# Kernel optimization log

Measured on AMD Instinct MI355X. Metric: run time of the kernel, lower is better.

Reference implementation:

```python
import jax, jax.numpy as jnp
import numpy as np

HIDDEN = 1024
HEADS = 16
HEAD_DIM = HIDDEN // HEADS


def setup_inputs() -> dict:
    key = jax.random.key(0)
    ks = jax.random.split(key, 7)
    B, S = 4, 2048
    xav = float(np.sqrt(6.0 / (HIDDEN + HIDDEN)))  # xavier uniform bound
    def lin(k):
        return jax.random.uniform(k, (HIDDEN, HIDDEN), jnp.float32, -xav, xav)
    return {
        "hidden_states": jax.random.normal(ks[0], (B, S, HIDDEN), jnp.float32),
        "Wq": lin(ks[1]), "bq": jnp.zeros((HIDDEN,), jnp.float32),
        "Wk": lin(ks[2]), "bk": jnp.zeros((HIDDEN,), jnp.float32),
        "Wv": lin(ks[3]), "bv": jnp.zeros((HIDDEN,), jnp.float32),
    }


def reference(hidden_states, Wq, bq, Wk, bk, Wv, bv):
    B, S, H = hidden_states.shape
    def split_heads(t):  # [B,S,H] -> [B,heads,S,head_dim]
        return t.reshape(B, S, HEADS, HEAD_DIM).transpose(0, 2, 1, 3)
    q = split_heads(hidden_states @ Wq + bq)
    k = split_heads(hidden_states @ Wk + bk)
    v = split_heads(hidden_states @ Wv + bv)
    scores = jnp.einsum("bhqd,bhkd->bhqk", q, k) / jnp.sqrt(
        jnp.asarray(HEAD_DIM, hidden_states.dtype))
    probs = jax.nn.softmax(scores, axis=-1)  # dropout p=0.0 (inference)
    ctx = jnp.einsum("bhqk,bhkd->bhqd", probs, v)
    ctx = ctx.transpose(0, 2, 1, 3).reshape(B, S, H)
    return ctx
```

## Files before the change

kernel.cpp:

```cpp
#include <hip/hip_runtime.h>
#include <hip/hip_bf16.h>
#include <cstdint>

#define HIDDEN 1024
#define HEADS 16
#define HDIM 64
#define BATCH 4
#define SEQ 2048
#define MTOT (BATCH * SEQ)

typedef __attribute__((ext_vector_type(8))) short bfrag;
typedef __attribute__((ext_vector_type(4))) float cfrag;
typedef __attribute__((ext_vector_type(4))) float float4v;
typedef __attribute__((ext_vector_type(4))) unsigned short ushort4v;
typedef __attribute__((ext_vector_type(2))) unsigned int uint2v;

#define AS1 __attribute__((address_space(1)))
#define AS3 __attribute__((address_space(3)))

__device__ __forceinline__ void gl_lds16(const void* g, void* l) {
  __builtin_amdgcn_global_load_lds((AS1 void*)g, (AS3 void*)l, 16, 0, 0);
}

__device__ __forceinline__ uint16_t f2b(float f) {
  union { float f; uint32_t u; } v; v.f = f;
  uint32_t u = v.u;
  return (uint16_t)((u + 0x7FFFu + ((u >> 16) & 1u)) >> 16);
}

__global__ __launch_bounds__(256) void cvt_x_kernel(const float* __restrict__ in,
                                                    uint16_t* __restrict__ out, int n8) {
  int i = blockIdx.x * blockDim.x + threadIdx.x;
  if (i >= n8) return;
  float4v a = ((const float4v*)in)[2 * i];
  float4v b = ((const float4v*)in)[2 * i + 1];
  bfrag o;
  o[0] = (short)f2b(a[0]); o[1] = (short)f2b(a[1]);
  o[2] = (short)f2b(a[2]); o[3] = (short)f2b(a[3]);
  o[4] = (short)f2b(b[0]); o[5] = (short)f2b(b[1]);
  o[6] = (short)f2b(b[2]); o[7] = (short)f2b(b[3]);
  ((bfrag*)out)[i] = o;
}

__global__ __launch_bounds__(256) void cvt_w_kernel(const float* __restrict__ W0,
                                                    const float* __restrict__ W1,
                                                    const float* __restrict__ W2,
                                                    uint16_t* __restrict__ Wt) {
  const float* W = blockIdx.z == 0 ? W0 : (blockIdx.z == 1 ? W1 : W2);
  uint16_t* out = Wt + (size_t)blockIdx.z * HIDDEN * HIDDEN;
  __shared__ float tile[64][65];
  int n0 = blockIdx.x * 64, k0 = blockIdx.y * 64;
  int t = threadIdx.x;
  int r = t >> 2, cq = (t & 3) * 16;
#pragma unroll
  for (int i = 0; i < 16; i += 4) {
    float4v v = *(const float4v*)&W[(size_t)(k0 + r) * HIDDEN + n0 + cq + i];
    tile[r][cq + i + 0] = v[0]; tile[r][cq + i + 1] = v[1];
    tile[r][cq + i + 2] = v[2]; tile[r][cq + i + 3] = v[3];
  }
  __syncthreads();
  bfrag o0, o1;
#pragma unroll
  for (int i = 0; i < 8; ++i) o0[i] = (short)f2b(tile[cq + i][r]);
#pragma unroll
  for (int i = 0; i < 8; ++i) o1[i] = (short)f2b(tile[cq + 8 + i][r]);
  *(bfrag*)&out[(size_t)(n0 + r) * HIDDEN + k0 + cq] = o0;
  *(bfrag*)&out[(size_t)(n0 + r) * HIDDEN + k0 + cq + 8] = o1;
}

__global__ __launch_bounds__(256) void gemm_qkv_kernel(
    const uint16_t* __restrict__ X, const uint16_t* __restrict__ Wt,
    const float* __restrict__ b0, const float* __restrict__ b1,
    const float* __restrict__ b2,
    uint16_t* __restrict__ Qo, uint16_t* __restrict__ Ko, uint16_t* __restrict__ Vo) {
  __shared__ uint16_t As[128 * 32];
  __shared__ uint16_t Bs[128 * 32];

  int id = blockIdx.x;
  int xcd = id & 7, j = id >> 3;
  int which = j >> 6;
  int r_ = j & 63;
  int m0 = (xcd * 8 + (r_ >> 3)) * 128;
  int n0 = (r_ & 7) * 128;

  const uint16_t* Wp = Wt + (size_t)which * HIDDEN * HIDDEN;
  const float* bias = which == 0 ? b0 : (which == 1 ? b1 : b2);

  int tid = threadIdx.x;
  int wave = tid >> 6, lane = tid & 63;
  int wm = wave >> 1, wn = wave & 1;
  int g = lane >> 4, c = lane & 15;
  int sr = lane >> 2;
  int sc = (lane & 3) * 8;

  cfrag acc[4][4];
#pragma unroll
  for (int i = 0; i < 4; ++i)
#pragma unroll
    for (int jj = 0; jj < 4; ++jj) acc[i][jj] = cfrag{0.f, 0.f, 0.f, 0.f};

  for (int kt = 0; kt < HIDDEN / 32; ++kt) {
    int kc = kt * 32 + sc;
#pragma unroll
    for (int i = 0; i < 2; ++i) {
      int rowA = (i * 4 + wave) * 16;
      gl_lds16(&X[(size_t)(m0 + rowA + sr) * HIDDEN + kc], &As[rowA * 32]);
      gl_lds16(&Wp[(size_t)(n0 + rowA + sr) * HIDDEN + kc], &Bs[rowA * 32]);
    }
    __syncthreads();
    bfrag af[4], bf[4];
#pragma unroll
    for (int mt = 0; mt < 4; ++mt)
      af[mt] = *(const bfrag*)&As[(wm * 64 + mt * 16 + c) * 32 + g * 8];
#pragma unroll
    for (int nt = 0; nt < 4; ++nt)
      bf[nt] = *(const bfrag*)&Bs[(wn * 64 + nt * 16 + c) * 32 + g * 8];
#pragma unroll
    for (int mt = 0; mt < 4; ++mt)
#pragma unroll
      for (int nt = 0; nt < 4; ++nt)
        acc[mt][nt] = __builtin_amdgcn_mfma_f32_16x16x32_bf16(af[mt], bf[nt],
                                                              acc[mt][nt], 0, 0, 0);
    __syncthreads();
  }

  if (which == 2) {
    int bb_ = m0 >> 11;
    int s0 = (m0 & 2047) + wm * 64;
#pragma unroll
    for (int nt = 0; nt < 4; ++nt) {
      int n = n0 + wn * 64 + nt * 16 + c;
      int h = n >> 6, d = n & 63;
      float bb = bias[n];
      size_t base = ((size_t)(bb_ * 16 + h) * 64 + d) * SEQ;
#pragma unroll
      for (int mt = 0; mt < 4; ++mt) {
        int s = s0 + mt * 16 + g * 4;
        ushort4v pk;
        pk[0] = f2b(acc[mt][nt][0] + bb);
        pk[1] = f2b(acc[mt][nt][1] + bb);
        pk[2] = f2b(acc[mt][nt][2] + bb);
        pk[3] = f2b(acc[mt][nt][3] + bb);
        *(ushort4v*)&Vo[base + s] = pk;
      }
    }
  } else {
    uint16_t* out = which == 0 ? Qo : Ko;
    float sc_ = which == 0 ? 0.125f * 1.44269504088896f : 1.0f;
#pragma unroll
    for (int nt = 0; nt < 4; ++nt) {
      int n = n0 + wn * 64 + nt * 16 + c;
      float bb = bias[n];
#pragma unroll
      for (int mt = 0; mt < 4; ++mt) {
        int mb = m0 + wm * 64 + mt * 16 + g * 4;
#pragma unroll
        for (int r = 0; r < 4; ++r)
          out[(size_t)(mb + r) * HIDDEN + n] = f2b((acc[mt][nt][r] + bb) * sc_);
      }
    }
  }
}

__global__ __launch_bounds__(256, 4) void attn_kernel(
    const uint16_t* __restrict__ Q, const uint16_t* __restrict__ K,
    const uint16_t* __restrict__ VT, float* __restrict__ out) {
  __shared__ uint16_t Ks[2][64 * 64];
  __shared__ uint16_t Vs[2][64 * 64];
  __shared__ __align__(16) uint16_t Pl[4][16][64];

  int bid = blockIdx.x;
  int wg = (bid & 7) * 256 + (bid >> 3);
  int bh = wg >> 5, qt = wg & 31;
  int b = bh >> 4, h = bh & 15;
  int tid = threadIdx.x, wave = tid >> 6, lane = tid & 63;
  int g = lane >> 4, c = lane & 15;
  size_t rowb = (size_t)b * SEQ;
  int colb = h * HDIM;
  const uint16_t* Kh = K + rowb * HIDDEN + colb;
  const uint16_t* Vh = VT + (size_t)bh * HDIM * SEQ;

  int r8 = lane >> 3, c8 = lane & 7;
  int scol = ((c8 ^ r8) << 3);
  int sbrow = (wave & 1) * 32;

  int qrow = qt * 64 + wave * 16 + c;
  bfrag aq[2];
  aq[0] = *(const bfrag*)&Q[(rowb + qrow) * HIDDEN + colb + g * 8];
  aq[1] = *(const bfrag*)&Q[(rowb + qrow) * HIDDEN + colb + 32 + g * 8];

  float mr = -INFINITY, lr = 0.f;
  cfrag oacc[4];
#pragma unroll
  for (int dt = 0; dt < 4; ++dt) oacc[dt] = cfrag{0.f, 0.f, 0.f, 0.f};

  if (wave < 2) {
#pragma unroll
    for (int j = 0; j < 4; ++j) {
      int rl = sbrow + j * 8;
      gl_lds16(&Kh[(size_t)(rl + r8) * HIDDEN + scol], &Ks[0][rl * 64]);
    }
  } else {
#pragma unroll
    for (int j = 0; j < 4; ++j) {
      int rl = sbrow + j * 8;
      gl_lds16(&Vh[(size_t)(rl + r8) * SEQ + scol], &Vs[0][rl * 64]);
    }
  }
  __syncthreads();

  int cur = 0;
  int sw = (c & 7) << 4;
  uint8_t* Pb = (uint8_t*)Pl + wave * 2048 + c * 128;

  for (int t = 0; t < 32; ++t) {
    int j0 = t * 64;
    if (t < 31) {
      int jn = j0 + 64;
      if (wave < 2) {
#pragma unroll
        for (int j = 0; j < 4; ++j) {
          int rl = sbrow + j * 8;
          gl_lds16(&Kh[(size_t)(jn + rl + r8) * HIDDEN + scol],
                   &Ks[cur ^ 1][rl * 64]);
        }
      } else {
#pragma unroll
        for (int j = 0; j < 4; ++j) {
          int rl = sbrow + j * 8;
          gl_lds16(&Vh[(size_t)(rl + r8) * SEQ + jn + scol],
                   &Vs[cur ^ 1][rl * 64]);
        }
      }
    }

    const uint8_t* Kbuf = (const uint8_t*)Ks[cur];
    const uint8_t* Vbuf = (const uint8_t*)Vs[cur];

    cfrag s[4];
#pragma unroll
    for (int nt = 0; nt < 4; ++nt) s[nt] = cfrag{0.f, 0.f, 0.f, 0.f};
    __builtin_amdgcn_s_setprio(1);
#pragma unroll
    for (int kb = 0; kb < 2; ++kb) {
#pragma unroll
      for (int nt = 0; nt < 4; ++nt) {
        int off = ((nt * 16 + c) * 128 + kb * 64 + g * 16) ^ sw;
        bfrag bk = *(const bfrag*)(Kbuf + off);
        s[nt] = __builtin_amdgcn_mfma_f32_16x16x32_bf16(bk, aq[kb], s[nt], 0, 0, 0);
      }
    }
    __builtin_amdgcn_s_setprio(0);

    float mx = fmaxf(fmaxf(fmaxf(s[0][0], s[0][1]), s[0][2]), s[0][3]);
    float mx1 = fmaxf(fmaxf(fmaxf(s[1][0], s[1][1]), s[1][2]), s[1][3]);
    float mx2 = fmaxf(fmaxf(fmaxf(s[2][0], s[2][1]), s[2][2]), s[2][3]);
    float mx3 = fmaxf(fmaxf(fmaxf(s[3][0], s[3][1]), s[3][2]), s[3][3]);
    mx = fmaxf(fmaxf(mx, mx1), fmaxf(mx2, mx3));
    mx = fmaxf(mx, __shfl_xor(mx, 16, 64));
    mx = fmaxf(mx, __shfl_xor(mx, 32, 64));
    if (mx > mr + 8.0f) {
      float alpha = __builtin_amdgcn_exp2f(mr - mx);
      lr *= alpha;
#pragma unroll
      for (int dt = 0; dt < 4; ++dt)
#pragma unroll
        for (int r = 0; r < 4; ++r) oacc[dt][r] *= alpha;
      mr = mx;
    }
    float ps = 0.f;
#pragma unroll
    for (int nt = 0; nt < 4; ++nt) {
#pragma unroll
      for (int r = 0; r < 4; ++r)
        s[nt][r] = __builtin_amdgcn_exp2f(s[nt][r] - mr);
      ps += (s[nt][0] + s[nt][1]) + (s[nt][2] + s[nt][3]);
    }
    lr += ps;

#pragma unroll
    for (int nt = 0; nt < 4; ++nt) {
      uint32_t w0, w1;
      asm("v_cvt_pk_bf16_f32 %0, %1, %2" : "=v"(w0) : "v"(s[nt][0]), "v"(s[nt][1]));
      asm("v_cvt_pk_bf16_f32 %0, %1, %2" : "=v"(w1) : "v"(s[nt][2]), "v"(s[nt][3]));
      uint2v pw; pw[0] = w0; pw[1] = w1;
      *(uint2v*)(Pb + ((nt * 32 + g * 8) ^ sw)) = pw;
    }

    __builtin_amdgcn_s_setprio(1);
#pragma unroll
    for (int kb = 0; kb < 2; ++kb) {
      bfrag ap = *(const bfrag*)(Pb + ((kb * 64 + g * 16) ^ sw));
#pragma unroll
      for (int dt = 0; dt < 4; ++dt) {
        int off = ((dt * 16 + c) * 128 + kb * 64 + g * 16) ^ sw;
        bfrag bv = *(const bfrag*)(Vbuf + off);
        oacc[dt] = __builtin_amdgcn_mfma_f32_16x16x32_bf16(bv, ap, oacc[dt], 0, 0, 0);
      }
    }
    __builtin_amdgcn_s_setprio(0);

    __syncthreads();
    cur ^= 1;
  }

  lr += __shfl_xor(lr, 16, 64);
  lr += __shfl_xor(lr, 32, 64);
  float inv = 1.0f / lr;
  size_t orow = rowb + (size_t)qt * 64 + wave * 16 + c;
#pragma unroll
  for (int dt = 0; dt < 4; ++dt) {
    float4v o;
    o[0] = oacc[dt][0] * inv; o[1] = oacc[dt][1] * inv;
    o[2] = oacc[dt][2] * inv; o[3] = oacc[dt][3] * inv;
    *(float4v*)&out[orow * HIDDEN + colb + dt * 16 + g * 4] = o;
  }
}

extern "C" void kernel_launch(void* const* d_in, const int* in_sizes, int n_in,
                              void* d_out, int out_size, void* d_ws, size_t ws_size,
                              hipStream_t stream) {
  const float* x  = (const float*)d_in[0];
  const float* Wq = (const float*)d_in[1];
  const float* bq = (const float*)d_in[2];
  const float* Wk = (const float*)d_in[3];
  const float* bk = (const float*)d_in[4];
  const float* Wv = (const float*)d_in[5];
  const float* bv = (const float*)d_in[6];
  float* out = (float*)d_out;

  uint8_t* ws = (uint8_t*)d_ws;
  const size_t XB = 0;
  const size_t WT = XB + (size_t)MTOT * HIDDEN * 2;
  const size_t QB = WT + (size_t)3 * HIDDEN * HIDDEN * 2;
  const size_t KB = QB + (size_t)MTOT * HIDDEN * 2;
  const size_t VB = KB + (size_t)MTOT * HIDDEN * 2;
  uint16_t* Xb = (uint16_t*)(ws + XB);
  uint16_t* Wt = (uint16_t*)(ws + WT);
  uint16_t* Qb = (uint16_t*)(ws + QB);
  uint16_t* Kb = (uint16_t*)(ws + KB);
  uint16_t* Vb = (uint16_t*)(ws + VB);

  cvt_x_kernel<<<dim3(MTOT * HIDDEN / 8 / 256), 256, 0, stream>>>(x, Xb,
                                                                  MTOT * HIDDEN / 8);
  cvt_w_kernel<<<dim3(16, 16, 3), 256, 0, stream>>>(Wq, Wk, Wv, Wt);
  gemm_qkv_kernel<<<dim3(1536), 256, 0, stream>>>(Xb, Wt, bq, bk, bv, Qb, Kb, Vb);
  attn_kernel<<<dim3(2048), 256, 0, stream>>>(Qb, Kb, Vb, out);
}
```

Before: 277.0 us.

## Merge conversion kernels, double-buffer QKV GEMM LDS, restructure softmax max reduction

The two fp32-to-bf16 conversion kernels are merged into one launch that picks its role by block index, removing one kernel launch and its tail. The QKV GEMM now double-buffers its LDS tiles, issuing the next k-tile's global-to-LDS load before computing on the current one, and raises wave priority around the MFMA block. The attention row-max is rewritten as a serial fmax chain. The double buffering doubles the GEMM's LDS use, which may lower occupancy. It also relies on one barrier per iteration to order the asynchronous LDS loads, which could be fragile.

Result: slower. 284.7 us (+2.8%).

```diff
diff --git a/kernel.cpp b/kernel.cpp
--- a/kernel.cpp
+++ b/kernel.cpp
@@ -28,28 +28,29 @@
   return (uint16_t)((u + 0x7FFFu + ((u >> 16) & 1u)) >> 16);
 }
 
-__global__ __launch_bounds__(256) void cvt_x_kernel(const float* __restrict__ in,
-                                                    uint16_t* __restrict__ out, int n8) {
-  int i = blockIdx.x * blockDim.x + threadIdx.x;
-  if (i >= n8) return;
-  float4v a = ((const float4v*)in)[2 * i];
-  float4v b = ((const float4v*)in)[2 * i + 1];
-  bfrag o;
-  o[0] = (short)f2b(a[0]); o[1] = (short)f2b(a[1]);
-  o[2] = (short)f2b(a[2]); o[3] = (short)f2b(a[3]);
-  o[4] = (short)f2b(b[0]); o[5] = (short)f2b(b[1]);
-  o[6] = (short)f2b(b[2]); o[7] = (short)f2b(b[3]);
-  ((bfrag*)out)[i] = o;
-}
-
-__global__ __launch_bounds__(256) void cvt_w_kernel(const float* __restrict__ W0,
-                                                    const float* __restrict__ W1,
-                                                    const float* __restrict__ W2,
-                                                    uint16_t* __restrict__ Wt) {
-  const float* W = blockIdx.z == 0 ? W0 : (blockIdx.z == 1 ? W1 : W2);
-  uint16_t* out = Wt + (size_t)blockIdx.z * HIDDEN * HIDDEN;
+__global__ __launch_bounds__(256) void cvt_kernel(
+    const float* __restrict__ x, const float* __restrict__ W0,
+    const float* __restrict__ W1, const float* __restrict__ W2,
+    uint16_t* __restrict__ Xb, uint16_t* __restrict__ Wt) {
+  int bid = blockIdx.x;
+  if (bid < 4096) {
+    int i = bid * 256 + threadIdx.x;
+    float4v a = ((const float4v*)x)[2 * i];
+    float4v b = ((const float4v*)x)[2 * i + 1];
+    bfrag o;
+    o[0] = (short)f2b(a[0]); o[1] = (short)f2b(a[1]);
+    o[2] = (short)f2b(a[2]); o[3] = (short)f2b(a[3]);
+    o[4] = (short)f2b(b[0]); o[5] = (short)f2b(b[1]);
+    o[6] = (short)f2b(b[2]); o[7] = (short)f2b(b[3]);
+    ((bfrag*)Xb)[i] = o;
+    return;
+  }
+  int id = bid - 4096;
+  int z = id >> 8, rem = id & 255;
+  const float* W = z == 0 ? W0 : (z == 1 ? W1 : W2);
+  uint16_t* out = Wt + (size_t)z * HIDDEN * HIDDEN;
   __shared__ float tile[64][65];
-  int n0 = blockIdx.x * 64, k0 = blockIdx.y * 64;
+  int n0 = (rem & 15) * 64, k0 = (rem >> 4) * 64;
   int t = threadIdx.x;
   int r = t >> 2, cq = (t & 3) * 16;
 #pragma unroll
@@ -73,8 +74,8 @@
     const float* __restrict__ b0, const float* __restrict__ b1,
     const float* __restrict__ b2,
     uint16_t* __restrict__ Qo, uint16_t* __restrict__ Ko, uint16_t* __restrict__ Vo) {
-  __shared__ uint16_t As[128 * 32];
-  __shared__ uint16_t Bs[128 * 32];
+  __shared__ uint16_t As[2][128 * 32];
+  __shared__ uint16_t Bs[2][128 * 32];
 
   int id = blockIdx.x;
   int xcd = id & 7, j = id >> 3;
@@ -99,29 +100,39 @@
 #pragma unroll
     for (int jj = 0; jj < 4; ++jj) acc[i][jj] = cfrag{0.f, 0.f, 0.f, 0.f};
 
-  for (int kt = 0; kt < HIDDEN / 32; ++kt) {
+  auto STAGE = [&](int buf, int kt) {
     int kc = kt * 32 + sc;
 #pragma unroll
     for (int i = 0; i < 2; ++i) {
       int rowA = (i * 4 + wave) * 16;
-      gl_lds16(&X[(size_t)(m0 + rowA + sr) * HIDDEN + kc], &As[rowA * 32]);
-      gl_lds16(&Wp[(size_t)(n0 + rowA + sr) * HIDDEN + kc], &Bs[rowA * 32]);
-    }
-    __syncthreads();
+      gl_lds16(&X[(size_t)(m0 + rowA + sr) * HIDDEN + kc], &As[buf][rowA * 32]);
+      gl_lds16(&Wp[(size_t)(n0 + rowA + sr) * HIDDEN + kc], &Bs[buf][rowA * 32]);
+    }
+  };
+
+  STAGE(0, 0);
+  __syncthreads();
+  int cur = 0;
+
+  for (int kt = 0; kt < HIDDEN / 32; ++kt) {
+    if (kt < HIDDEN / 32 - 1) STAGE(cur ^ 1, kt + 1);
     bfrag af[4], bf[4];
 #pragma unroll
     for (int mt = 0; mt < 4; ++mt)
-      af[mt] = *(const bfrag*)&As[(wm * 64 + mt * 16 + c) * 32 + g * 8];
+      af[mt] = *(const bfrag*)&As[cur][(wm * 64 + mt * 16 + c) * 32 + g * 8];
 #pragma unroll
     for (int nt = 0; nt < 4; ++nt)
-      bf[nt] = *(const bfrag*)&Bs[(wn * 64 + nt * 16 + c) * 32 + g * 8];
+      bf[nt] = *(const bfrag*)&Bs[cur][(wn * 64 + nt * 16 + c) * 32 + g * 8];
+    __builtin_amdgcn_s_setprio(1);
 #pragma unroll
     for (int mt = 0; mt < 4; ++mt)
 #pragma unroll
       for (int nt = 0; nt < 4; ++nt)
         acc[mt][nt] = __builtin_amdgcn_mfma_f32_16x16x32_bf16(af[mt], bf[nt],
                                                               acc[mt][nt], 0, 0, 0);
+    __builtin_amdgcn_s_setprio(0);
     __syncthreads();
+    cur ^= 1;
   }
 
   if (which == 2) {
@@ -252,11 +263,14 @@
     }
     __builtin_amdgcn_s_setprio(0);
 
-    float mx = fmaxf(fmaxf(fmaxf(s[0][0], s[0][1]), s[0][2]), s[0][3]);
-    float mx1 = fmaxf(fmaxf(fmaxf(s[1][0], s[1][1]), s[1][2]), s[1][3]);
-    float mx2 = fmaxf(fmaxf(fmaxf(s[2][0], s[2][1]), s[2][2]), s[2][3]);
-    float mx3 = fmaxf(fmaxf(fmaxf(s[3][0], s[3][1]), s[3][2]), s[3][3]);
-    mx = fmaxf(fmaxf(mx, mx1), fmaxf(mx2, mx3));
+    float mx = fmaxf(fmaxf(s[0][0], s[0][1]), s[0][2]);
+    mx = fmaxf(fmaxf(mx, s[0][3]), s[1][0]);
+    mx = fmaxf(fmaxf(mx, s[1][1]), s[1][2]);
+    mx = fmaxf(fmaxf(mx, s[1][3]), s[2][0]);
+    mx = fmaxf(fmaxf(mx, s[2][1]), s[2][2]);
+    mx = fmaxf(fmaxf(mx, s[2][3]), s[3][0]);
+    mx = fmaxf(fmaxf(mx, s[3][1]), s[3][2]);
+    mx = fmaxf(mx, s[3][3]);
     mx = fmaxf(mx, __shfl_xor(mx, 16, 64));
     mx = fmaxf(mx, __shfl_xor(mx, 32, 64));
     if (mx > mr + 8.0f) {
@@ -341,9 +355,7 @@
   uint16_t* Kb = (uint16_t*)(ws + KB);
   uint16_t* Vb = (uint16_t*)(ws + VB);
 
-  cvt_x_kernel<<<dim3(MTOT * HIDDEN / 8 / 256), 256, 0, stream>>>(x, Xb,
-                                                                  MTOT * HIDDEN / 8);
-  cvt_w_kernel<<<dim3(16, 16, 3), 256, 0, stream>>>(Wq, Wk, Wv, Wt);
+  cvt_kernel<<<dim3(4096 + 768), 256, 0, stream>>>(x, Wq, Wk, Wv, Xb, Wt);
   gemm_qkv_kernel<<<dim3(1536), 256, 0, stream>>>(Xb, Wt, bq, bk, bv, Qb, Kb, Vb);
   attn_kernel<<<dim3(2048), 256, 0, stream>>>(Qb, Kb, Vb, out);
 }
```
